# Performance work log

Hardware: AMD Instinct MI355X
Metric: run time of the kernel (lower is better)

## Reference

```python
import jax, jax.numpy as jnp
import numpy as np

EMBED_DIM = 1024
NUM_HEADS = 16
HEAD_DIM = EMBED_DIM // NUM_HEADS
BATCH = 2
SEQ = 2048


def setup_inputs() -> dict:
    key = jax.random.key(0)
    ks = jax.random.split(key, 9)
    s = 1.0 / np.sqrt(EMBED_DIM)
    return {
        "x": jax.random.normal(ks[0], (BATCH, SEQ, EMBED_DIM), jnp.float32),
        "mask": jnp.ones((BATCH, SEQ), jnp.int32),
        "Wq": jax.random.normal(ks[1], (EMBED_DIM, EMBED_DIM), jnp.float32) * s,
        "bq": jax.random.normal(ks[2], (EMBED_DIM,), jnp.float32) * s,
        "Wk": jax.random.normal(ks[3], (EMBED_DIM, EMBED_DIM), jnp.float32) * s,
        "bk": jax.random.normal(ks[4], (EMBED_DIM,), jnp.float32) * s,
        "Wv": jax.random.normal(ks[5], (EMBED_DIM, EMBED_DIM), jnp.float32) * s,
        "bv": jax.random.normal(ks[6], (EMBED_DIM,), jnp.float32) * s,
        "Wo": jax.random.normal(ks[7], (EMBED_DIM, EMBED_DIM), jnp.float32) * s,
        "bo": jax.random.normal(ks[8], (EMBED_DIM,), jnp.float32) * s,
    }


def reference(x, mask, Wq, bq, Wk, bk, Wv, bv, Wo, bo):
    B, S, E = x.shape
    H, D = NUM_HEADS, HEAD_DIM
    # torch Linear: y = x @ W.T + b
    q = (x @ Wq.T + bq).reshape(B, S, H, D).transpose(0, 2, 1, 3)  # [B,H,S,D]
    k = (x @ Wk.T + bk).reshape(B, S, H, D).transpose(0, 2, 1, 3)
    v = (x @ Wv.T + bv).reshape(B, S, H, D).transpose(0, 2, 1, 3)
    scores = jnp.einsum("bhqd,bhkd->bhqk", q, k) / jnp.sqrt(jnp.float32(D))
    # mask: [B,S] -> [B,1,1,S]; fill masked positions with -1e9
    scores = jnp.where(mask[:, None, None, :] == 0, jnp.float32(-1e9), scores)
    probs = jax.nn.softmax(scores, axis=-1)
    # dropout omitted: original stores a float and would crash; eval semantics = identity
    attn = jnp.einsum("bhqk,bhkd->bhqd", probs, v)  # [B,H,S,D]
    attn = attn.transpose(0, 2, 1, 3).reshape(B, S, E)
    return attn @ Wo.T + bo
```

## Files before the change

kernel.cpp:

```cpp
#include <hip/hip_runtime.h>
#include <stdint.h>

#define S_LEN 2048
#define EMB   1024
#define NH    16
#define HD    64
#define BK 64

typedef __bf16 bf16x8 __attribute__((ext_vector_type(8)));
typedef short  short4v __attribute__((ext_vector_type(4)));
typedef unsigned int uint2v __attribute__((ext_vector_type(2)));
typedef float  floatx4 __attribute__((ext_vector_type(4)));

#if defined(__has_builtin)
#if __has_builtin(__builtin_amdgcn_mfma_f32_16x16x16bf16_1k)
#define HAVE_MFMA16 1
#endif
#if __has_builtin(__builtin_amdgcn_exp2f)
#define EXP2F __builtin_amdgcn_exp2f
#endif
#endif
#ifndef EXP2F
#define EXP2F exp2f
#endif

#define QSCALE 0.1803368801111204f

__device__ __forceinline__ unsigned short f2bf(float f) {
  unsigned u = __builtin_bit_cast(unsigned, f);
  u += 0x7fffu + ((u >> 16) & 1u);
  return (unsigned short)(u >> 16);
}
__device__ __forceinline__ unsigned short f2bf_hu(float f) {
  return (unsigned short)((__builtin_bit_cast(unsigned, f) + 0x8000u) >> 16);
}
__device__ __forceinline__ unsigned packbf2(float a, float b) {
  unsigned ua = __builtin_bit_cast(unsigned, a) + 0x8000u;
  unsigned ub = __builtin_bit_cast(unsigned, b) + 0x8000u;
  return __builtin_amdgcn_perm(ub, ua, 0x07060302);
}

__global__ __launch_bounds__(256) void cvt_all(const float* __restrict__ x,
                                               const float* __restrict__ Wq,
                                               const float* __restrict__ Wk,
                                               const float* __restrict__ Wv,
                                               const float* __restrict__ Wo,
                                               unsigned short* __restrict__ xb,
                                               unsigned short* __restrict__ Wqb,
                                               unsigned short* __restrict__ Wkb,
                                               unsigned short* __restrict__ Wvb,
                                               unsigned short* __restrict__ Wob) {
  int blk = blockIdx.x;
  const float* s; unsigned short* d; int off;
  if (blk < 4096)      { s = x;  d = xb;  off = blk; }
  else if (blk < 5120) { s = Wq; d = Wqb; off = blk - 4096; }
  else if (blk < 6144) { s = Wk; d = Wkb; off = blk - 5120; }
  else if (blk < 7168) { s = Wv; d = Wvb; off = blk - 6144; }
  else                 { s = Wo; d = Wob; off = blk - 7168; }
  int i = (off * 256 + threadIdx.x) * 4;
  float4 v = *(const float4*)(s + i);
  ushort4 o;
  o.x = f2bf(v.x); o.y = f2bf(v.y); o.z = f2bf(v.z); o.w = f2bf(v.w);
  *(ushort4*)(d + i) = o;
}

__device__ __forceinline__ void stage16(const void* g, void* l) {
  __builtin_amdgcn_global_load_lds(
      (const __attribute__((address_space(1))) void*)g,
      (__attribute__((address_space(3))) void*)l, 16, 0, 0);
}

__global__ __launch_bounds__(256, 4) void qkv_gemm(const unsigned short* __restrict__ xb,
                                                   const unsigned short* __restrict__ Wqb,
                                                   const unsigned short* __restrict__ Wkb,
                                                   const unsigned short* __restrict__ Wvb,
                                                   const float* __restrict__ bq,
                                                   const float* __restrict__ bk,
                                                   const float* __restrict__ bv,
                                                   unsigned short* __restrict__ Qb,
                                                   unsigned short* __restrict__ Kb,
                                                   unsigned short* __restrict__ Vtb) {
  __shared__ unsigned short As[64 * BK];
  __shared__ unsigned short Bs[128 * BK];
  const int z = blockIdx.z;
  const unsigned short* Bm = (z == 0) ? Wqb : (z == 1) ? Wkb : Wvb;
  const float* bias        = (z == 0) ? bq  : (z == 1) ? bk  : bv;
  unsigned short* outp     = (z == 0) ? Qb  : (z == 1) ? Kb  : Vtb;
  const float scale = (z == 0) ? QSCALE : 1.0f;
  const int mode = (z == 2) ? 2 : 1;

  const int tid  = threadIdx.x;
  const int lane = tid & 63;
  const int wave = tid >> 6;
  const int m16  = lane & 15;
  const int quad = lane >> 4;
  const int m0 = blockIdx.x * 64;
  const int n0 = blockIdx.y * 128;
  const int wrow = (wave >> 1) * 32;
  const int wcol = (wave & 1) * 64;
  const int K = 1024;

  floatx4 acc[2][4];
  for (int i = 0; i < 2; ++i)
    for (int j = 0; j < 4; ++j) acc[i][j] = floatx4{0.f, 0.f, 0.f, 0.f};

  for (int k0 = 0; k0 < K; k0 += BK) {
    __syncthreads();
    for (int i = 0; i < 2; ++i) {
      int c = i * 256 + tid;
      int row = c >> 3, col = (c & 7) << 3;
      stage16(xb + (size_t)(m0 + row) * K + k0 + col,
              (char*)As + (size_t)(i * 256 + wave * 64) * 16);
    }
    for (int i = 0; i < 4; ++i) {
      int c = i * 256 + tid;
      int row = c >> 3, col = (c & 7) << 3;
      stage16(Bm + (size_t)(n0 + row) * K + k0 + col,
              (char*)Bs + (size_t)(i * 256 + wave * 64) * 16);
    }
    __syncthreads();
    for (int kk = 0; kk < 2; ++kk) {
      bf16x8 af[2], bfr[4];
      for (int ti = 0; ti < 2; ++ti)
        af[ti] = *(const bf16x8*)(As + (wrow + ti * 16 + m16) * BK + kk * 32 + quad * 8);
      for (int tj = 0; tj < 4; ++tj)
        bfr[tj] = *(const bf16x8*)(Bs + (wcol + tj * 16 + m16) * BK + kk * 32 + quad * 8);
      for (int ti = 0; ti < 2; ++ti)
        for (int tj = 0; tj < 4; ++tj)
          acc[ti][tj] = __builtin_amdgcn_mfma_f32_16x16x32_bf16(bfr[tj], af[ti], acc[ti][tj], 0, 0, 0);
    }
  }

  if (mode == 1) {
    for (int ti = 0; ti < 2; ++ti) {
      int m = m0 + wrow + ti * 16 + m16;
      int b = m >> 11, ss = m & 2047;
      for (int tj = 0; tj < 4; ++tj) {
        int n = n0 + wcol + tj * 16 + quad * 4;
        int hh = n >> 6, d = n & 63;
        float4 b4 = *(const float4*)(bias + n);
        float v0 = (acc[ti][tj][0] + b4.x) * scale;
        float v1 = (acc[ti][tj][1] + b4.y) * scale;
        float v2 = (acc[ti][tj][2] + b4.z) * scale;
        float v3 = (acc[ti][tj][3] + b4.w) * scale;
        uint2v pk{packbf2(v0, v1), packbf2(v2, v3)};
        *(uint2v*)((unsigned short*)outp +
                   ((size_t)(b * NH + hh) * S_LEN + ss) * HD + d) = pk;
      }
    }
  } else {
    for (int tj = 0; tj < 4; ++tj)
      for (int reg = 0; reg < 4; ++reg) {
        int n = n0 + wcol + tj * 16 + quad * 4 + reg;
        int hh = n >> 6, d = n & 63;
        float bv = bias[n];
        for (int ti = 0; ti < 2; ++ti) {
          int m = m0 + wrow + ti * 16 + m16;
          int b = m >> 11, ss = m & 2047;
          ((unsigned short*)outp)[((size_t)(b * NH + hh) * HD + d) * S_LEN + ss] =
              f2bf_hu(acc[ti][tj][reg] + bv);
        }
      }
  }
}

__global__ __launch_bounds__(256, 4) void out_gemm(const unsigned short* __restrict__ Ab,
                                                   const unsigned short* __restrict__ Wob,
                                                   const float* __restrict__ bo,
                                                   float* __restrict__ out) {
  __shared__ unsigned short As[64 * BK];
  __shared__ unsigned short Bs[64 * BK];
  const int tid  = threadIdx.x;
  const int lane = tid & 63;
  const int wave = tid >> 6;
  const int m16  = lane & 15;
  const int quad = lane >> 4;
  const int m0 = blockIdx.x * 64;
  const int n0 = blockIdx.y * 64;
  const int wrow = (wave >> 1) * 32;
  const int wcol = (wave & 1) * 32;
  const int K = 1024, N = 1024;

  floatx4 acc[2][2];
  for (int i = 0; i < 2; ++i)
    for (int j = 0; j < 2; ++j) acc[i][j] = floatx4{0.f, 0.f, 0.f, 0.f};

  for (int k0 = 0; k0 < K; k0 += BK) {
    __syncthreads();
    for (int i = 0; i < 2; ++i) {
      int c = i * 256 + tid;
      int row = c >> 3, col = (c & 7) << 3;
      stage16(Ab + (size_t)(m0 + row) * K + k0 + col,
              (char*)As + (size_t)(i * 256 + wave * 64) * 16);
      stage16(Wob + (size_t)(n0 + row) * K + k0 + col,
              (char*)Bs + (size_t)(i * 256 + wave * 64) * 16);
    }
    __syncthreads();
    for (int kk = 0; kk < 2; ++kk) {
      bf16x8 af[2], bfr[2];
      for (int ti = 0; ti < 2; ++ti)
        af[ti] = *(const bf16x8*)(As + (wrow + ti * 16 + m16) * BK + kk * 32 + quad * 8);
      for (int tj = 0; tj < 2; ++tj)
        bfr[tj] = *(const bf16x8*)(Bs + (wcol + tj * 16 + m16) * BK + kk * 32 + quad * 8);
      for (int ti = 0; ti < 2; ++ti)
        for (int tj = 0; tj < 2; ++tj)
          acc[ti][tj] = __builtin_amdgcn_mfma_f32_16x16x32_bf16(af[ti], bfr[tj], acc[ti][tj], 0, 0, 0);
    }
  }

  for (int tj = 0; tj < 2; ++tj) {
    int n = n0 + wcol + tj * 16 + m16;
    float bv = bo[n];
    for (int ti = 0; ti < 2; ++ti)
      for (int reg = 0; reg < 4; ++reg) {
        int m = m0 + wrow + ti * 16 + quad * 4 + reg;
        out[(size_t)m * N + n] = acc[ti][tj][reg] + bv;
      }
  }
}

__global__ __launch_bounds__(512, 2) void attn_kernel(const unsigned short* __restrict__ Qb,
                                                      const unsigned short* __restrict__ Kb,
                                                      const unsigned short* __restrict__ Vtb,
                                                      const int* __restrict__ mask,
                                                      unsigned short* __restrict__ attnb) {
  __shared__ unsigned short Ks[2 * 128 * 64];
  __shared__ unsigned short Vts[2 * 64 * 128];
  __shared__ int zw[8];
#ifndef HAVE_MFMA16
  __shared__ unsigned short Pq[8 * 16 * 72];
#endif

  const int tid  = threadIdx.x;
  const int lane = tid & 63;
  const int wave = tid >> 6;
  const int m16  = lane & 15;
  const int quad = lane >> 4;
  const int bh = blockIdx.x;
  const int qt = blockIdx.y;
  const int b  = bh >> 4;
  const int h  = bh & 15;
  const int q0 = qt * 128;
  const size_t head = (size_t)bh * S_LEN * HD;

  bf16x8 qf[2];
  {
    const unsigned short* qrow = Qb + head + (size_t)(q0 + wave * 16 + m16) * HD;
    qf[0] = *(const bf16x8*)(qrow + quad * 8);
    qf[1] = *(const bf16x8*)(qrow + 32 + quad * 8);
  }

  const int krow = tid >> 3, kch = tid & 7;
  const unsigned short* kg = Kb + head + (size_t)krow * HD + kch * 8;
  const int kloff = krow * 64 + ((kch ^ (krow & 7)) << 3);
  const int vrow = tid >> 4, vch = tid & 15;
  const unsigned short* vg = Vtb + head + (size_t)vrow * S_LEN + vch * 8;
  const int vloff = vrow * 128 + ((vch ^ (vrow & 7)) << 3);
  const int* mrow = mask + b * S_LEN;

  float l_run = 0.f;
  floatx4 acc_o[4];
  for (int ti = 0; ti < 4; ++ti) acc_o[ti] = floatx4{0.f, 0.f, 0.f, 0.f};

  {
    int4 mv = *(const int4*)(mrow + tid * 4);
    bool z = (mv.x & mv.y & mv.z & mv.w) == 0;
    unsigned long long bal = __ballot(z);
    if (lane == 0) zw[wave] = (bal != 0ull) ? 1 : 0;
  }

  uint4 kp0 = *(const uint4*)(kg);
  uint4 kp1 = *(const uint4*)(kg + 64 * HD);
  uint4 vp0 = *(const uint4*)(vg);
  uint4 vp1 = *(const uint4*)(vg + 32 * S_LEN);
  *(uint4*)&Ks[kloff] = kp0;  *(uint4*)&Ks[64 * 64 + kloff] = kp1;
  *(uint4*)&Vts[vloff] = vp0; *(uint4*)&Vts[32 * 128 + vloff] = vp1;
  kp0 = *(const uint4*)(kg + 128 * HD);
  kp1 = *(const uint4*)(kg + 192 * HD);
  vp0 = *(const uint4*)(vg + 128);
  vp1 = *(const uint4*)(vg + 32 * S_LEN + 128);
  __syncthreads();
  const bool anymask = (zw[0] | zw[1] | zw[2] | zw[3] | zw[4] | zw[5] | zw[6] | zw[7]) != 0;

  const int xs = m16 & 7;
  const floatx4 fz = floatx4{0.f, 0.f, 0.f, 0.f};

  for (int kb = 0; kb < 16; ++kb) {
    const int p = kb & 1;
    const unsigned short* Kp = Ks + p * (128 * 64);
    const unsigned short* Vp = Vts + p * (64 * 128);
    if (kb < 15) {
      unsigned short* Kn = Ks + (p ^ 1) * (128 * 64);
      unsigned short* Vn = Vts + (p ^ 1) * (64 * 128);
      *(uint4*)&Kn[kloff] = kp0;  *(uint4*)&Kn[64 * 64 + kloff] = kp1;
      *(uint4*)&Vn[vloff] = vp0;  *(uint4*)&Vn[32 * 128 + vloff] = vp1;
      int kvn = (kb + 2 < 16) ? (kb + 2) * 128 : 0;
      kp0 = *(const uint4*)(kg + (size_t)kvn * HD);
      kp1 = *(const uint4*)(kg + (size_t)(kvn + 64) * HD);
      vp0 = *(const uint4*)(vg + kvn);
      vp1 = *(const uint4*)(vg + 32 * S_LEN + kvn);
    }

    for (int hf = 0; hf < 2; ++hf) {
      floatx4 acc_s[4];
      for (int tj = 0; tj < 4; ++tj) {
        bf16x8 kf0 = *(const bf16x8*)&Kp[(hf * 64 + tj * 16 + m16) * 64 + ((quad ^ xs) << 3)];
        acc_s[tj] = __builtin_amdgcn_mfma_f32_16x16x32_bf16(kf0, qf[0], fz, 0, 0, 0);
      }
      for (int tj = 0; tj < 4; ++tj) {
        bf16x8 kf1 = *(const bf16x8*)&Kp[(hf * 64 + tj * 16 + m16) * 64 + (((4 + quad) ^ xs) << 3)];
        acc_s[tj] = __builtin_amdgcn_mfma_f32_16x16x32_bf16(kf1, qf[1], acc_s[tj], 0, 0, 0);
      }

      float sv[16];
      for (int t = 0; t < 4; ++t)
        for (int r = 0; r < 4; ++r) sv[t * 4 + r] = acc_s[t][r];
      if (anymask) {
        for (int t = 0; t < 4; ++t)
          for (int r = 0; r < 4; ++r) {
            int idx = kb * 128 + hf * 64 + t * 16 + quad * 4 + r;
            sv[t * 4 + r] += (mrow[idx] == 0) ? -1e9f : 0.f;
          }
      }

      unsigned up[8];
      float sl = 0.f;
      for (int i = 0; i < 8; ++i) {
        float p0 = EXP2F(sv[2 * i]);
        float p1 = EXP2F(sv[2 * i + 1]);
        sl += p0 + p1;
        up[i] = packbf2(p0, p1);
      }
      sl += __shfl_xor(sl, 16);
      sl += __shfl_xor(sl, 32);
      l_run += sl;

#ifdef HAVE_MFMA16
      for (int ti = 0; ti < 4; ++ti)
        for (int c = 0; c < 4; ++c) {
          short4v vf = *(const short4v*)&Vp[(ti * 16 + m16) * 128 +
                                            (((hf * 8 + 2 * c + (quad >> 1)) ^ xs) << 3) +
                                            ((quad & 1) << 2)];
          short4v Pb = __builtin_bit_cast(short4v, uint2v{up[2 * c], up[2 * c + 1]});
          acc_o[ti] = __builtin_amdgcn_mfma_f32_16x16x16bf16_1k(vf, Pb, acc_o[ti], 0, 0, 0);
        }
#else
      unsigned short* Pw = Pq + wave * 16 * 72;
      for (int t = 0; t < 4; ++t) {
        *(unsigned*)&Pw[m16 * 72 + t * 16 + quad * 4]     = up[2 * t];
        *(unsigned*)&Pw[m16 * 72 + t * 16 + quad * 4 + 2] = up[2 * t + 1];
      }
      for (int kk = 0; kk < 2; ++kk) {
        bf16x8 pf = *(const bf16x8*)&Pw[m16 * 72 + kk * 32 + quad * 8];
        for (int ti = 0; ti < 4; ++ti) {
          bf16x8 vf = *(const bf16x8*)&Vp[(ti * 16 + m16) * 128 +
                                          (((hf * 8 + kk * 4 + quad) ^ xs) << 3)];
          acc_o[ti] = __builtin_amdgcn_mfma_f32_16x16x32_bf16(vf, pf, acc_o[ti], 0, 0, 0);
        }
      }
#endif
    }

    __syncthreads();
  }

  float rl = 1.f / l_run;
  int orow = q0 + wave * 16 + m16;
  for (int ti = 0; ti < 4; ++ti) {
    ushort4 o;
    o.x = f2bf_hu(acc_o[ti][0] * rl);
    o.y = f2bf_hu(acc_o[ti][1] * rl);
    o.z = f2bf_hu(acc_o[ti][2] * rl);
    o.w = f2bf_hu(acc_o[ti][3] * rl);
    int e = h * HD + ti * 16 + quad * 4;
    *(ushort4*)&attnb[((size_t)(b * S_LEN + orow)) * EMB + e] = o;
  }
}

extern "C" void kernel_launch(void* const* d_in, const int* in_sizes, int n_in,
                              void* d_out, int out_size, void* d_ws, size_t ws_size,
                              hipStream_t stream) {
  const float* x  = (const float*)d_in[0];
  const int* mask = (const int*)d_in[1];
  const float* Wq = (const float*)d_in[2];
  const float* bq = (const float*)d_in[3];
  const float* Wk = (const float*)d_in[4];
  const float* bk = (const float*)d_in[5];
  const float* Wv = (const float*)d_in[6];
  const float* bv = (const float*)d_in[7];
  const float* Wo = (const float*)d_in[8];
  const float* bo = (const float*)d_in[9];
  float* out = (float*)d_out;

  char* ws = (char*)d_ws;
  unsigned short* xb  = (unsigned short*)(ws);
  unsigned short* Wqb = (unsigned short*)(ws + 8388608);
  unsigned short* Wkb = (unsigned short*)(ws + 10485760);
  unsigned short* Wvb = (unsigned short*)(ws + 12582912);
  unsigned short* Wob = (unsigned short*)(ws + 14680064);
  unsigned short* Qb  = (unsigned short*)(ws + 16777216);
  unsigned short* Kbb = (unsigned short*)(ws + 25165824);
  unsigned short* Vtb = (unsigned short*)(ws + 33554432);
  unsigned short* Ab  = (unsigned short*)(ws + 41943040);

  cvt_all<<<dim3(8192), dim3(256), 0, stream>>>(x, Wq, Wk, Wv, Wo, xb, Wqb, Wkb, Wvb, Wob);
  qkv_gemm<<<dim3(64, 8, 3), dim3(256), 0, stream>>>(xb, Wqb, Wkb, Wvb, bq, bk, bv, Qb, Kbb, Vtb);
  attn_kernel<<<dim3(32, 16), dim3(512), 0, stream>>>(Qb, Kbb, Vtb, mask, Ab);
  out_gemm<<<dim3(64, 16), dim3(256), 0, stream>>>(Ab, Wob, bo, out);
}
```

Measured before the change: 210.4 us.

## Halve attention KV tile to 64 keys and raise occupancy launch bounds

Shrinks the attention kernel's double-buffered K and V shared-memory tiles from 128 to 64 keys per step and doubles the loop trip count. Each thread now stages a single uint4 per tensor instead of two. Launch bounds are raised for both the attention kernel (2 to 8) and the output GEMM (4 to 6), so more blocks can be resident to hide latency. In exchange there are twice as many block-wide barriers, and the compiler faces tighter register limits that could cause spills.

```diff
diff --git a/kernel.cpp b/kernel.cpp
--- a/kernel.cpp
+++ b/kernel.cpp
@@ -164,7 +164,7 @@
   }
 }
 
-__global__ __launch_bounds__(256, 4) void out_gemm(const unsigned short* __restrict__ Ab,
+__global__ __launch_bounds__(256, 6) void out_gemm(const unsigned short* __restrict__ Ab,
                                                    const unsigned short* __restrict__ Wob,
                                                    const float* __restrict__ bo,
                                                    float* __restrict__ out) {
@@ -219,13 +219,13 @@
   }
 }
 
-__global__ __launch_bounds__(512, 2) void attn_kernel(const unsigned short* __restrict__ Qb,
+__global__ __launch_bounds__(512, 8) void attn_kernel(const unsigned short* __restrict__ Qb,
                                                       const unsigned short* __restrict__ Kb,
                                                       const unsigned short* __restrict__ Vtb,
                                                       const int* __restrict__ mask,
                                                       unsigned short* __restrict__ attnb) {
-  __shared__ unsigned short Ks[2 * 128 * 64];
-  __shared__ unsigned short Vts[2 * 64 * 128];
+  __shared__ unsigned short Ks[2 * 64 * 64];
+  __shared__ unsigned short Vts[2 * 64 * 64];
   __shared__ int zw[8];
 #ifndef HAVE_MFMA16
   __shared__ unsigned short Pq[8 * 16 * 72];
@@ -250,12 +250,10 @@
     qf[1] = *(const bf16x8*)(qrow + 32 + quad * 8);
   }
 
-  const int krow = tid >> 3, kch = tid & 7;
-  const unsigned short* kg = Kb + head + (size_t)krow * HD + kch * 8;
-  const int kloff = krow * 64 + ((kch ^ (krow & 7)) << 3);
-  const int vrow = tid >> 4, vch = tid & 15;
-  const unsigned short* vg = Vtb + head + (size_t)vrow * S_LEN + vch * 8;
-  const int vloff = vrow * 128 + ((vch ^ (vrow & 7)) << 3);
+  const int srow = tid >> 3, sch = tid & 7;
+  const unsigned short* kg = Kb + head + (size_t)srow * HD + sch * 8;
+  const unsigned short* vg = Vtb + head + (size_t)srow * S_LEN + sch * 8;
+  const int sloff = srow * 64 + ((sch ^ (srow & 7)) << 3);
   const int* mrow = mask + b * S_LEN;
 
   float l_run = 0.f;
@@ -269,97 +267,88 @@
     if (lane == 0) zw[wave] = (bal != 0ull) ? 1 : 0;
   }
 
-  uint4 kp0 = *(const uint4*)(kg);
-  uint4 kp1 = *(const uint4*)(kg + 64 * HD);
-  uint4 vp0 = *(const uint4*)(vg);
-  uint4 vp1 = *(const uint4*)(vg + 32 * S_LEN);
-  *(uint4*)&Ks[kloff] = kp0;  *(uint4*)&Ks[64 * 64 + kloff] = kp1;
-  *(uint4*)&Vts[vloff] = vp0; *(uint4*)&Vts[32 * 128 + vloff] = vp1;
-  kp0 = *(const uint4*)(kg + 128 * HD);
-  kp1 = *(const uint4*)(kg + 192 * HD);
-  vp0 = *(const uint4*)(vg + 128);
-  vp1 = *(const uint4*)(vg + 32 * S_LEN + 128);
+  uint4 kp = *(const uint4*)(kg);
+  uint4 vp = *(const uint4*)(vg);
+  *(uint4*)&Ks[sloff] = kp;
+  *(uint4*)&Vts[sloff] = vp;
+  kp = *(const uint4*)(kg + 64 * HD);
+  vp = *(const uint4*)(vg + 64);
   __syncthreads();
   const bool anymask = (zw[0] | zw[1] | zw[2] | zw[3] | zw[4] | zw[5] | zw[6] | zw[7]) != 0;
 
   const int xs = m16 & 7;
   const floatx4 fz = floatx4{0.f, 0.f, 0.f, 0.f};
 
-  for (int kb = 0; kb < 16; ++kb) {
+  for (int kb = 0; kb < 32; ++kb) {
     const int p = kb & 1;
-    const unsigned short* Kp = Ks + p * (128 * 64);
-    const unsigned short* Vp = Vts + p * (64 * 128);
-    if (kb < 15) {
-      unsigned short* Kn = Ks + (p ^ 1) * (128 * 64);
-      unsigned short* Vn = Vts + (p ^ 1) * (64 * 128);
-      *(uint4*)&Kn[kloff] = kp0;  *(uint4*)&Kn[64 * 64 + kloff] = kp1;
-      *(uint4*)&Vn[vloff] = vp0;  *(uint4*)&Vn[32 * 128 + vloff] = vp1;
-      int kvn = (kb + 2 < 16) ? (kb + 2) * 128 : 0;
-      kp0 = *(const uint4*)(kg + (size_t)kvn * HD);
-      kp1 = *(const uint4*)(kg + (size_t)(kvn + 64) * HD);
-      vp0 = *(const uint4*)(vg + kvn);
-      vp1 = *(const uint4*)(vg + 32 * S_LEN + kvn);
-    }
-
-    for (int hf = 0; hf < 2; ++hf) {
-      floatx4 acc_s[4];
-      for (int tj = 0; tj < 4; ++tj) {
-        bf16x8 kf0 = *(const bf16x8*)&Kp[(hf * 64 + tj * 16 + m16) * 64 + ((quad ^ xs) << 3)];
-        acc_s[tj] = __builtin_amdgcn_mfma_f32_16x16x32_bf16(kf0, qf[0], fz, 0, 0, 0);
-      }
-      for (int tj = 0; tj < 4; ++tj) {
-        bf16x8 kf1 = *(const bf16x8*)&Kp[(hf * 64 + tj * 16 + m16) * 64 + (((4 + quad) ^ xs) << 3)];
-        acc_s[tj] = __builtin_amdgcn_mfma_f32_16x16x32_bf16(kf1, qf[1], acc_s[tj], 0, 0, 0);
-      }
-
-      float sv[16];
+    const unsigned short* Kp = Ks + p * (64 * 64);
+    const unsigned short* Vp = Vts + p * (64 * 64);
+    if (kb < 31) {
+      unsigned short* Kn = Ks + (p ^ 1) * (64 * 64);
+      unsigned short* Vn = Vts + (p ^ 1) * (64 * 64);
+      *(uint4*)&Kn[sloff] = kp;
+      *(uint4*)&Vn[sloff] = vp;
+      int kvn = (kb + 2 < 32) ? (kb + 2) * 64 : 0;
+      kp = *(const uint4*)(kg + (size_t)kvn * HD);
+      vp = *(const uint4*)(vg + kvn);
+    }
+
+    floatx4 acc_s[4];
+    for (int tj = 0; tj < 4; ++tj) {
+      bf16x8 kf0 = *(const bf16x8*)&Kp[(tj * 16 + m16) * 64 + ((quad ^ xs) << 3)];
+      acc_s[tj] = __builtin_amdgcn_mfma_f32_16x16x32_bf16(kf0, qf[0], fz, 0, 0, 0);
+    }
+    for (int tj = 0; tj < 4; ++tj) {
+      bf16x8 kf1 = *(const bf16x8*)&Kp[(tj * 16 + m16) * 64 + (((4 + quad) ^ xs) << 3)];
+      acc_s[tj] = __builtin_amdgcn_mfma_f32_16x16x32_bf16(kf1, qf[1], acc_s[tj], 0, 0, 0);
+    }
+
+    float sv[16];
+    for (int t = 0; t < 4; ++t)
+      for (int r = 0; r < 4; ++r) sv[t * 4 + r] = acc_s[t][r];
+    if (anymask) {
       for (int t = 0; t < 4; ++t)
-        for (int r = 0; r < 4; ++r) sv[t * 4 + r] = acc_s[t][r];
-      if (anymask) {
-        for (int t = 0; t < 4; ++t)
-          for (int r = 0; r < 4; ++r) {
-            int idx = kb * 128 + hf * 64 + t * 16 + quad * 4 + r;
-            sv[t * 4 + r] += (mrow[idx] == 0) ? -1e9f : 0.f;
-          }
-      }
-
-      unsigned up[8];
-      float sl = 0.f;
-      for (int i = 0; i < 8; ++i) {
-        float p0 = EXP2F(sv[2 * i]);
-        float p1 = EXP2F(sv[2 * i + 1]);
-        sl += p0 + p1;
-        up[i] = packbf2(p0, p1);
-      }
-      sl += __shfl_xor(sl, 16);
-      sl += __shfl_xor(sl, 32);
-      l_run += sl;
+        for (int r = 0; r < 4; ++r) {
+          int idx = kb * 64 + t * 16 + quad * 4 + r;
+          sv[t * 4 + r] += (mrow[idx] == 0) ? -1e9f : 0.f;
+        }
+    }
+
+    unsigned up[8];
+    float sl = 0.f;
+    for (int i = 0; i < 8; ++i) {
+      float p0 = EXP2F(sv[2 * i]);
+      float p1 = EXP2F(sv[2 * i + 1]);
+      sl += p0 + p1;
+      up[i] = packbf2(p0, p1);
+    }
+    sl += __shfl_xor(sl, 16);
+    sl += __shfl_xor(sl, 32);
+    l_run += sl;
 
 #ifdef HAVE_MFMA16
-      for (int ti = 0; ti < 4; ++ti)
-        for (int c = 0; c < 4; ++c) {
-          short4v vf = *(const short4v*)&Vp[(ti * 16 + m16) * 128 +
-                                            (((hf * 8 + 2 * c + (quad >> 1)) ^ xs) << 3) +
-                                            ((quad & 1) << 2)];
-          short4v Pb = __builtin_bit_cast(short4v, uint2v{up[2 * c], up[2 * c + 1]});
-          acc_o[ti] = __builtin_amdgcn_mfma_f32_16x16x16bf16_1k(vf, Pb, acc_o[ti], 0, 0, 0);
-        }
+    for (int ti = 0; ti < 4; ++ti)
+      for (int c = 0; c < 4; ++c) {
+        short4v vf = *(const short4v*)&Vp[(ti * 16 + m16) * 64 +
+                                          (((2 * c + (quad >> 1)) ^ xs) << 3) +
+                                          ((quad & 1) << 2)];
+        short4v Pb = __builtin_bit_cast(short4v, uint2v{up[2 * c], up[2 * c + 1]});
+        acc_o[ti] = __builtin_amdgcn_mfma_f32_16x16x16bf16_1k(vf, Pb, acc_o[ti], 0, 0, 0);
+      }
 #else
-      unsigned short* Pw = Pq + wave * 16 * 72;
-      for (int t = 0; t < 4; ++t) {
-        *(unsigned*)&Pw[m16 * 72 + t * 16 + quad * 4]     = up[2 * t];
-        *(unsigned*)&Pw[m16 * 72 + t * 16 + quad * 4 + 2] = up[2 * t + 1];
-      }
-      for (int kk = 0; kk < 2; ++kk) {
-        bf16x8 pf = *(const bf16x8*)&Pw[m16 * 72 + kk * 32 + quad * 8];
-        for (int ti = 0; ti < 4; ++ti) {
-          bf16x8 vf = *(const bf16x8*)&Vp[(ti * 16 + m16) * 128 +
-                                          (((hf * 8 + kk * 4 + quad) ^ xs) << 3)];
-          acc_o[ti] = __builtin_amdgcn_mfma_f32_16x16x32_bf16(vf, pf, acc_o[ti], 0, 0, 0);
-        }
-      }
-#endif
-    }
+    unsigned short* Pw = Pq + wave * 16 * 72;
+    for (int t = 0; t < 4; ++t) {
+      *(unsigned*)&Pw[m16 * 72 + t * 16 + quad * 4]     = up[2 * t];
+      *(unsigned*)&Pw[m16 * 72 + t * 16 + quad * 4 + 2] = up[2 * t + 1];
+    }
+    for (int kk = 0; kk < 2; ++kk) {
+      bf16x8 pf = *(const bf16x8*)&Pw[m16 * 72 + kk * 32 + quad * 8];
+      for (int ti = 0; ti < 4; ++ti) {
+        bf16x8 vf = *(const bf16x8*)&Vp[(ti * 16 + m16) * 64 + (((kk * 4 + quad) ^ xs) << 3)];
+        acc_o[ti] = __builtin_amdgcn_mfma_f32_16x16x32_bf16(vf, pf, acc_o[ti], 0, 0, 0);
+      }
+    }
+#endif
 
     __syncthreads();
   }
```

After: 294.9 us. +40.2%, slower.
